# Kernel tuning notes

Hardware: AMD Instinct MI355X
Metric: run time of the kernel (lower is better)

## Reference

```python
import jax, jax.numpy as jnp
import numpy as np

B, S, D_ENC, D_DEC, UNITS = 64, 2048, 512, 512, 512


def setup_inputs() -> dict:
    key = jax.random.key(0)
    ks = jax.random.split(key, 8)
    enc = jax.random.normal(ks[0], (B, S, D_ENC), dtype=jnp.float32)
    dec = jax.random.normal(ks[1], (B, D_DEC), dtype=jnp.float32)
    # Dense params (glorot-ish scale)
    W1 = jax.random.normal(ks[2], (D_ENC, UNITS), dtype=jnp.float32) / np.sqrt(D_ENC)
    b1 = jnp.zeros((UNITS,), dtype=jnp.float32)
    W2 = jax.random.normal(ks[3], (D_DEC, UNITS), dtype=jnp.float32) / np.sqrt(D_DEC)
    b2 = jnp.zeros((UNITS,), dtype=jnp.float32)
    V = jax.random.normal(ks[4], (UNITS, 1), dtype=jnp.float32) / np.sqrt(UNITS)
    bv = jnp.zeros((1,), dtype=jnp.float32)
    return {"encoder_outputs": enc, "decoder_hidden": dec,
            "W1": W1, "b1": b1, "W2": W2, "b2": b2, "V": V, "bv": bv}


def reference(encoder_outputs, decoder_hidden, W1, b1, W2, b2, V, bv):
    # score_features: [B,S,U] = tanh(W1(enc) + W2(dec)[:,None,:])
    proj_enc = jnp.einsum('bsd,du->bsu', encoder_outputs, W1) + b1
    proj_dec = decoder_hidden @ W2 + b2                      # [B,U]
    feat = jnp.tanh(proj_enc + proj_dec[:, None, :])         # [B,S,U]
    score = jnp.einsum('bsu,uo->bso', feat, V) + bv          # [B,S,1]
    attn = jax.nn.softmax(score, axis=1)                     # softmax over seq
    context = jnp.sum(attn * encoder_outputs, axis=1)        # [B,D_enc]
    return context, jnp.squeeze(attn, axis=-1)
```

## Files before the change

### kernel.cpp

```cpp
#include <hip/hip_runtime.h>
#include <hip/hip_bf16.h>

#define BATCH 64
#define SEQ   2048
#define DIM   512
#define MROWS (BATCH * SEQ)

typedef short bf16x8 __attribute__((ext_vector_type(8)));
typedef float f32x4  __attribute__((ext_vector_type(4)));

static __device__ __forceinline__ unsigned short f2bf(float f) {
    union { float f; unsigned u; } v; v.f = f;
    unsigned u = v.u;
    u += 0x7FFFu + ((u >> 16) & 1u);
    return (unsigned short)(u >> 16);
}
static __device__ __forceinline__ float bf2f(unsigned short h) {
    union { unsigned u; float f; } v; v.u = ((unsigned)h) << 16; return v.f;
}

static __device__ __forceinline__ float tanh_fast(float x) {
    float xc = fminf(20.0f, fmaxf(-20.0f, x));
#if __has_builtin(__builtin_amdgcn_exp2f)
    float t = __builtin_amdgcn_exp2f(2.885390082f * xc);
#else
    float t = exp2f(2.885390082f * xc);
#endif
#if __has_builtin(__builtin_amdgcn_rcpf)
    return (t - 1.0f) * __builtin_amdgcn_rcpf(t + 1.0f);
#else
    return (t - 1.0f) / (t + 1.0f);
#endif
}

typedef __attribute__((address_space(1))) const unsigned int gu32;
typedef __attribute__((address_space(3))) unsigned int lu32;
static __device__ __forceinline__ void gload_lds16(const unsigned short* g,
                                                   unsigned short* l) {
    __builtin_amdgcn_global_load_lds((gu32*)g, (lu32*)l, 16, 0, 0);
}

__global__ void prep_w1t_kernel(const float* __restrict__ W1,
                                unsigned short* __restrict__ w1t) {
    int stride = gridDim.x * blockDim.x;
    for (int i = blockIdx.x * blockDim.x + threadIdx.x; i < DIM * DIM; i += stride) {
        int k = i >> 9;
        int u = i & 511;
        w1t[u * DIM + k] = f2bf(W1[i]);
    }
}

__global__ void conv_enc_kernel(const float* __restrict__ enc,
                                unsigned short* __restrict__ encb) {
    const size_t nunits = (size_t)MROWS * DIM / 8;
    size_t stride = (size_t)gridDim.x * blockDim.x;
    for (size_t u = (size_t)blockIdx.x * blockDim.x + threadIdx.x; u < nunits;
         u += stride) {
        const float4* p = (const float4*)(enc + u * 8);
        float4 a = p[0], b = p[1];
        union { ushort4 s[2]; uint4 q; } o;
        o.s[0].x = f2bf(a.x); o.s[0].y = f2bf(a.y);
        o.s[0].z = f2bf(a.z); o.s[0].w = f2bf(a.w);
        o.s[1].x = f2bf(b.x); o.s[1].y = f2bf(b.y);
        o.s[1].z = f2bf(b.z); o.s[1].w = f2bf(b.w);
        *(uint4*)(encb + u * 8) = o.q;
    }
}

__global__ void proj_dec_kernel(const float* __restrict__ dec,
                                const float* __restrict__ W2,
                                const float* __restrict__ b1,
                                const float* __restrict__ b2,
                                float* __restrict__ pd) {
    __shared__ float sdec[DIM];
    const int b = blockIdx.x;
    const int t = threadIdx.x;
    sdec[t]       = dec[b * DIM + t];
    sdec[t + 256] = dec[b * DIM + t + 256];
    __syncthreads();
    const int u0 = t, u1 = t + 256;
    float a0 = b1[u0] + b2[u0];
    float a1 = b1[u1] + b2[u1];
    for (int k = 0; k < DIM; ++k) {
        float dk = sdec[k];
        a0 += dk * W2[k * DIM + u0];
        a1 += dk * W2[k * DIM + u1];
    }
    pd[b * DIM + u0] = a0;
    pd[b * DIM + u1] = a1;
}

#define BM3 64
#define BK3 64

__global__ __launch_bounds__(256, 2) void gemm_score_v3(
    const unsigned short* __restrict__ encb,
    const unsigned short* __restrict__ w1t,
    const float* __restrict__ pd,
    const float* __restrict__ V,
    float* __restrict__ scores)
{
    __shared__ unsigned short sA[BM3 * BK3];
    __shared__ unsigned short sB[DIM * BK3];

    const int tid  = threadIdx.x;
    const int lane = tid & 63;
    const int wave = tid >> 6;
    const int quad = lane >> 4;
    const int l15  = lane & 15;

    const int row0 = blockIdx.x * BM3;

    f32x4 acc[8][4];
    for (int j = 0; j < 8; ++j)
        for (int tr = 0; tr < 4; ++tr)
            acc[j][tr] = (f32x4){0.f, 0.f, 0.f, 0.f};

    for (int k0 = 0; k0 < DIM; k0 += BK3) {
        for (int i = 0; i < 2; ++i) {
            int c  = i * 256 + tid;
            int r  = c >> 3;
            int cc = c & 7;
            int gc = cc ^ (r & 7);
            gload_lds16(encb + (size_t)(row0 + r) * DIM + k0 + gc * 8, &sA[c * 8]);
        }
        for (int i = 0; i < 16; ++i) {
            int c  = i * 256 + tid;
            int r  = c >> 3;
            int cc = c & 7;
            int gc = cc ^ (r & 7);
            gload_lds16(w1t + (size_t)r * DIM + k0 + gc * 8, &sB[c * 8]);
        }
        __syncthreads();

        for (int kk = 0; kk < BK3; kk += 32) {
            int jc = (kk >> 3) + quad;
            bf16x8 af[4];
            for (int tr = 0; tr < 4; ++tr) {
                int am = tr * 16 + l15;
                af[tr] = *(const bf16x8*)(&sA[am * BK3 + ((jc ^ (am & 7)) * 8)]);
            }
            for (int j = 0; j < 8; ++j) {
                int u = wave * 128 + j * 16 + l15;
                bf16x8 bfr = *(const bf16x8*)(&sB[u * BK3 + ((jc ^ (u & 7)) * 8)]);
                for (int tr = 0; tr < 4; ++tr)
                    acc[j][tr] = __builtin_amdgcn_mfma_f32_16x16x32_bf16(
                        af[tr], bfr, acc[j][tr], 0, 0, 0);
            }
        }
        __syncthreads();
    }

    const int b = row0 >> 11;
    float sacc[4][4];
    for (int tr = 0; tr < 4; ++tr)
        for (int r = 0; r < 4; ++r) sacc[tr][r] = 0.f;

    for (int j = 0; j < 8; ++j) {
        int u_g   = wave * 128 + j * 16 + l15;
        float pdv = pd[b * DIM + u_g];
        float vv  = V[u_g];
        for (int tr = 0; tr < 4; ++tr)
            for (int r = 0; r < 4; ++r)
                sacc[tr][r] += tanh_fast(acc[j][tr][r] + pdv) * vv;
    }
    for (int tr = 0; tr < 4; ++tr)
        for (int r = 0; r < 4; ++r) {
            float v = sacc[tr][r];
            v += __shfl_xor(v, 1);
            v += __shfl_xor(v, 2);
            v += __shfl_xor(v, 4);
            v += __shfl_xor(v, 8);
            sacc[tr][r] = v;
        }
    float* red = (float*)sA;
    if (l15 == 0) {
        for (int tr = 0; tr < 4; ++tr)
            for (int r = 0; r < 4; ++r)
                red[wave * BM3 + tr * 16 + quad * 4 + r] = sacc[tr][r];
    }
    __syncthreads();
    if (tid < BM3) {
        float s = red[tid] + red[BM3 + tid] + red[2 * BM3 + tid] + red[3 * BM3 + tid];
        scores[row0 + tid] = s;
    }
}

#define BM 128
#define BN 128
#define BK 64
#define SAS 72
__global__ __launch_bounds__(256, 2) void gemm_score_kernel(
    const float* __restrict__ enc,
    const unsigned short* __restrict__ w1t,
    const float* __restrict__ pd,
    const float* __restrict__ V,
    float* __restrict__ scores)
{
    __shared__ unsigned short sA[BM * SAS];
    __shared__ unsigned short sB[BN * SAS];

    const int tid  = threadIdx.x;
    const int lane = tid & 63;
    const int wave = tid >> 6;
    const int wm   = wave & 1;
    const int wn   = wave >> 1;
    const int quad = lane >> 4;
    const int l15  = lane & 15;

    const int row0 = blockIdx.x * BM;
    const int col0 = blockIdx.y * BN;

    f32x4 acc[4][4];
    for (int i = 0; i < 4; ++i)
        for (int j = 0; j < 4; ++j)
            acc[i][j] = (f32x4){0.f, 0.f, 0.f, 0.f};

    for (int k0 = 0; k0 < DIM; k0 += BK) {
        for (int i = 0; i < 8; ++i) {
            int s  = i * 256 + tid;
            int r  = s >> 4;
            int c4 = s & 15;
            const float4 v = *(const float4*)(enc + (size_t)(row0 + r) * DIM + k0 + c4 * 4);
            ushort4 p;
            p.x = f2bf(v.x); p.y = f2bf(v.y); p.z = f2bf(v.z); p.w = f2bf(v.w);
            *(ushort4*)(&sA[r * SAS + c4 * 4]) = p;
        }
        for (int i = 0; i < 4; ++i) {
            int s  = i * 256 + tid;
            int u  = s >> 3;
            int c8 = s & 7;
            const uint4 w = *(const uint4*)(w1t + (size_t)(col0 + u) * DIM + k0 + c8 * 8);
            *(uint4*)(&sB[u * SAS + c8 * 8]) = w;
        }
        __syncthreads();

        for (int kk = 0; kk < BK; kk += 32) {
            bf16x8 af[4], bfr[4];
            for (int t4 = 0; t4 < 4; ++t4) {
                int am = wm * 64 + t4 * 16 + l15;
                af[t4]  = *(const bf16x8*)(&sA[am * SAS + kk + quad * 8]);
                int bn = wn * 64 + t4 * 16 + l15;
                bfr[t4] = *(const bf16x8*)(&sB[bn * SAS + kk + quad * 8]);
            }
            for (int tr = 0; tr < 4; ++tr)
                for (int tc = 0; tc < 4; ++tc)
                    acc[tr][tc] = __builtin_amdgcn_mfma_f32_16x16x32_bf16(
                        af[tr], bfr[tc], acc[tr][tc], 0, 0, 0);
        }
        __syncthreads();
    }

    const int b = row0 >> 11;
    float sacc[4][4];
    for (int tr = 0; tr < 4; ++tr)
        for (int r = 0; r < 4; ++r) sacc[tr][r] = 0.f;

    for (int tc = 0; tc < 4; ++tc) {
        int u_g   = col0 + wn * 64 + tc * 16 + l15;
        float pdv = pd[b * DIM + u_g];
        float vv  = V[u_g];
        for (int tr = 0; tr < 4; ++tr)
            for (int r = 0; r < 4; ++r)
                sacc[tr][r] += tanh_fast(acc[tr][tc][r] + pdv) * vv;
    }
    for (int tr = 0; tr < 4; ++tr)
        for (int r = 0; r < 4; ++r) {
            float v = sacc[tr][r];
            v += __shfl_xor(v, 1);
            v += __shfl_xor(v, 2);
            v += __shfl_xor(v, 4);
            v += __shfl_xor(v, 8);
            sacc[tr][r] = v;
        }
    if (l15 == 0) {
        for (int tr = 0; tr < 4; ++tr)
            for (int r = 0; r < 4; ++r) {
                int m_g = row0 + wm * 64 + tr * 16 + quad * 4 + r;
                atomicAdd(&scores[m_g], sacc[tr][r]);
            }
    }
}

__global__ void softmax_kernel(const float* __restrict__ scores,
                               float* __restrict__ attn) {
    __shared__ float se[SEQ];
    __shared__ float red[256];
    const int b = blockIdx.x;
    const int t = threadIdx.x;
    const float* sc = scores + (size_t)b * SEQ;

    float v[8];
    float mx = -1e30f;
    for (int i = 0; i < 8; ++i) {
        v[i] = sc[t + i * 256];
        mx = fmaxf(mx, v[i]);
    }
    red[t] = mx;
    __syncthreads();
    for (int off = 128; off > 0; off >>= 1) {
        if (t < off) red[t] = fmaxf(red[t], red[t + off]);
        __syncthreads();
    }
    mx = red[0];
    __syncthreads();

    float sum = 0.f;
    for (int i = 0; i < 8; ++i) {
        float e = expf(v[i] - mx);
        se[t + i * 256] = e;
        sum += e;
    }
    red[t] = sum;
    __syncthreads();
    for (int off = 128; off > 0; off >>= 1) {
        if (t < off) red[t] += red[t + off];
        __syncthreads();
    }
    const float inv = 1.0f / red[0];
    for (int i = 0; i < 8; ++i)
        attn[(size_t)b * SEQ + t + i * 256] = se[t + i * 256] * inv;
}

#define SCHUNK 64
__global__ void context_fast(const unsigned short* __restrict__ encb,
                             const float* __restrict__ attn,
                             float* __restrict__ ctx) {
    __shared__ float sa[SCHUNK];
    __shared__ float sred[256 * 8];
    const int c = blockIdx.x;
    const int b = blockIdx.y;
    const int t = threadIdx.x;
    if (t < SCHUNK) sa[t] = attn[(size_t)b * SEQ + c * SCHUNK + t];
    __syncthreads();
    const int j2 = t >> 6;
    const int d0 = (t & 63) * 8;
    float a[8];
    for (int q = 0; q < 8; ++q) a[q] = 0.f;
    const unsigned short* base = encb + ((size_t)b * SEQ + (size_t)c * SCHUNK) * DIM;
    for (int it = 0; it < SCHUNK / 4; ++it) {
        int j = it * 4 + j2;
        float w = sa[j];
        bf16x8 v = *(const bf16x8*)(base + (size_t)j * DIM + d0);
        for (int q = 0; q < 8; ++q)
            a[q] += w * bf2f((unsigned short)v[q]);
    }
    for (int q = 0; q < 8; ++q) sred[t * 8 + q] = a[q];
    __syncthreads();
    if (t < 64) {
        for (int q = 0; q < 8; ++q) {
            float s = sred[t * 8 + q] + sred[(t + 64) * 8 + q] +
                      sred[(t + 128) * 8 + q] + sred[(t + 192) * 8 + q];
            atomicAdd(&ctx[b * DIM + t * 8 + q], s);
        }
    }
}

__global__ void context_kernel(const float* __restrict__ enc,
                               const float* __restrict__ attn,
                               float* __restrict__ ctx) {
    __shared__ float sa[SCHUNK];
    const int c = blockIdx.x;
    const int b = blockIdx.y;
    const int t = threadIdx.x;
    if (t < SCHUNK) sa[t] = attn[(size_t)b * SEQ + c * SCHUNK + t];
    __syncthreads();
    float a0 = 0.f, a1 = 0.f;
    const float* base = enc + ((size_t)b * SEQ + (size_t)c * SCHUNK) * DIM;
    for (int j = 0; j < SCHUNK; ++j) {
        float w = sa[j];
        a0 += w * base[(size_t)j * DIM + t];
        a1 += w * base[(size_t)j * DIM + t + 256];
    }
    atomicAdd(&ctx[b * DIM + t], a0);
    atomicAdd(&ctx[b * DIM + t + 256], a1);
}

extern "C" void kernel_launch(void* const* d_in, const int* in_sizes, int n_in,
                              void* d_out, int out_size, void* d_ws, size_t ws_size,
                              hipStream_t stream) {
    const float* enc = (const float*)d_in[0];
    const float* dec = (const float*)d_in[1];
    const float* W1  = (const float*)d_in[2];
    const float* b1  = (const float*)d_in[3];
    const float* W2  = (const float*)d_in[4];
    const float* b2  = (const float*)d_in[5];
    const float* V   = (const float*)d_in[6];

    float* out  = (float*)d_out;
    float* ctx  = out;
    float* attn = out + BATCH * DIM;

    const size_t ENCB_BYTES = (size_t)MROWS * DIM * 2;
    const size_t need = ENCB_BYTES + 131072 + 524288 + 524288;

    char* ws = (char*)d_ws;

    if (ws_size >= need) {
        unsigned short* encb = (unsigned short*)ws;
        float* pd            = (float*)(ws + ENCB_BYTES);
        unsigned short* w1t  = (unsigned short*)(ws + ENCB_BYTES + 131072);
        float* scores        = (float*)(ws + ENCB_BYTES + 131072 + 524288);

        hipMemsetAsync(ctx, 0, (size_t)BATCH * DIM * 4, stream);

        prep_w1t_kernel<<<256, 256, 0, stream>>>(W1, w1t);
        proj_dec_kernel<<<BATCH, 256, 0, stream>>>(dec, W2, b1, b2, pd);
        conv_enc_kernel<<<4096, 256, 0, stream>>>(enc, encb);
        gemm_score_v3<<<MROWS / BM3, 256, 0, stream>>>(encb, w1t, pd, V, scores);
        softmax_kernel<<<BATCH, 256, 0, stream>>>(scores, attn);
        context_fast<<<dim3(SEQ / SCHUNK, BATCH), 256, 0, stream>>>(encb, attn, ctx);
    } else {
        float* pd            = (float*)ws;
        unsigned short* w1t  = (unsigned short*)(ws + 131072);
        float* scores        = (float*)(ws + 131072 + 524288);

        hipMemsetAsync(scores, 0, (size_t)MROWS * 4, stream);
        hipMemsetAsync(ctx, 0, (size_t)BATCH * DIM * 4, stream);

        prep_w1t_kernel<<<256, 256, 0, stream>>>(W1, w1t);
        proj_dec_kernel<<<BATCH, 256, 0, stream>>>(dec, W2, b1, b2, pd);
        gemm_score_kernel<<<dim3(MROWS / BM, DIM / BN), 256, 0, stream>>>(
            enc, w1t, pd, V, scores);
        softmax_kernel<<<BATCH, 256, 0, stream>>>(scores, attn);
        context_kernel<<<dim3(SEQ / SCHUNK, BATCH), 256, 0, stream>>>(enc, attn, ctx);
    }
}
```

Baseline: 559.2 us.

## Fuse bf16 conversion into score GEMM and softmax into context kernel

```diff
diff --git a/kernel.cpp b/kernel.cpp
--- a/kernel.cpp
+++ b/kernel.cpp
@@ -14,9 +14,6 @@
     unsigned u = v.u;
     u += 0x7FFFu + ((u >> 16) & 1u);
     return (unsigned short)(u >> 16);
-}
-static __device__ __forceinline__ float bf2f(unsigned short h) {
-    union { unsigned u; float f; } v; v.u = ((unsigned)h) << 16; return v.f;
 }
 
 static __device__ __forceinline__ float tanh_fast(float x) {
@@ -50,51 +47,40 @@
     }
 }
 
-__global__ void conv_enc_kernel(const float* __restrict__ enc,
-                                unsigned short* __restrict__ encb) {
-    const size_t nunits = (size_t)MROWS * DIM / 8;
-    size_t stride = (size_t)gridDim.x * blockDim.x;
-    for (size_t u = (size_t)blockIdx.x * blockDim.x + threadIdx.x; u < nunits;
-         u += stride) {
-        const float4* p = (const float4*)(enc + u * 8);
-        float4 a = p[0], b = p[1];
-        union { ushort4 s[2]; uint4 q; } o;
-        o.s[0].x = f2bf(a.x); o.s[0].y = f2bf(a.y);
-        o.s[0].z = f2bf(a.z); o.s[0].w = f2bf(a.w);
-        o.s[1].x = f2bf(b.x); o.s[1].y = f2bf(b.y);
-        o.s[1].z = f2bf(b.z); o.s[1].w = f2bf(b.w);
-        *(uint4*)(encb + u * 8) = o.q;
-    }
-}
-
-__global__ void proj_dec_kernel(const float* __restrict__ dec,
-                                const float* __restrict__ W2,
-                                const float* __restrict__ b1,
-                                const float* __restrict__ b2,
-                                float* __restrict__ pd) {
+__global__ void proj_dec_v2(const float* __restrict__ dec,
+                            const float* __restrict__ W2,
+                            const float* __restrict__ b1,
+                            const float* __restrict__ b2,
+                            float* __restrict__ pd) {
     __shared__ float sdec[DIM];
-    const int b = blockIdx.x;
-    const int t = threadIdx.x;
+    __shared__ float red[4 * 64];
+    const int ug = blockIdx.x;
+    const int b  = blockIdx.y;
+    const int t  = threadIdx.x;
     sdec[t]       = dec[b * DIM + t];
     sdec[t + 256] = dec[b * DIM + t + 256];
     __syncthreads();
-    const int u0 = t, u1 = t + 256;
-    float a0 = b1[u0] + b2[u0];
-    float a1 = b1[u1] + b2[u1];
-    for (int k = 0; k < DIM; ++k) {
-        float dk = sdec[k];
-        a0 += dk * W2[k * DIM + u0];
-        a1 += dk * W2[k * DIM + u1];
-    }
-    pd[b * DIM + u0] = a0;
-    pd[b * DIM + u1] = a1;
+    const int u  = ug * 64 + (t & 63);
+    const int kq = t >> 6;
+    float acc = 0.f;
+    #pragma unroll 4
+    for (int k = kq * 128; k < kq * 128 + 128; ++k)
+        acc += sdec[k] * W2[k * DIM + u];
+    red[kq * 64 + (t & 63)] = acc;
+    __syncthreads();
+    if (t < 64) {
+        int u_g = ug * 64 + t;
+        float s = red[t] + red[64 + t] + red[128 + t] + red[192 + t]
+                + b1[u_g] + b2[u_g];
+        pd[b * DIM + u_g] = s;
+    }
 }
 
 #define BM3 64
 #define BK3 64
 
-__global__ __launch_bounds__(256, 2) void gemm_score_v3(
-    const unsigned short* __restrict__ encb,
+__global__ __launch_bounds__(256, 2) void gemm_score_v4(
+    const float* __restrict__ enc,
     const unsigned short* __restrict__ w1t,
     const float* __restrict__ pd,
     const float* __restrict__ V,
@@ -117,19 +103,26 @@
             acc[j][tr] = (f32x4){0.f, 0.f, 0.f, 0.f};
 
     for (int k0 = 0; k0 < DIM; k0 += BK3) {
-        for (int i = 0; i < 2; ++i) {
-            int c  = i * 256 + tid;
-            int r  = c >> 3;
-            int cc = c & 7;
-            int gc = cc ^ (r & 7);
-            gload_lds16(encb + (size_t)(row0 + r) * DIM + k0 + gc * 8, &sA[c * 8]);
-        }
         for (int i = 0; i < 16; ++i) {
             int c  = i * 256 + tid;
             int r  = c >> 3;
             int cc = c & 7;
             int gc = cc ^ (r & 7);
             gload_lds16(w1t + (size_t)r * DIM + k0 + gc * 8, &sB[c * 8]);
+        }
+        for (int i = 0; i < 2; ++i) {
+            int c  = i * 256 + tid;
+            int r  = c >> 3;
+            int cc = c & 7;
+            const float4* p =
+                (const float4*)(enc + (size_t)(row0 + r) * DIM + k0 + cc * 8);
+            float4 va = p[0], vb = p[1];
+            union { ushort4 s[2]; uint4 q; } o;
+            o.s[0].x = f2bf(va.x); o.s[0].y = f2bf(va.y);
+            o.s[0].z = f2bf(va.z); o.s[0].w = f2bf(va.w);
+            o.s[1].x = f2bf(vb.x); o.s[1].y = f2bf(vb.y);
+            o.s[1].z = f2bf(vb.z); o.s[1].w = f2bf(vb.w);
+            *(uint4*)(&sA[r * BK3 + ((cc ^ (r & 7)) * 8)]) = o.q;
         }
         __syncthreads();
 
@@ -186,110 +179,18 @@
     }
 }
 
-#define BM 128
-#define BN 128
-#define BK 64
-#define SAS 72
-__global__ __launch_bounds__(256, 2) void gemm_score_kernel(
+__global__ __launch_bounds__(256) void softmax_context_kernel(
+    const float* __restrict__ scores,
     const float* __restrict__ enc,
-    const unsigned short* __restrict__ w1t,
-    const float* __restrict__ pd,
-    const float* __restrict__ V,
-    float* __restrict__ scores)
-{
-    __shared__ unsigned short sA[BM * SAS];
-    __shared__ unsigned short sB[BN * SAS];
-
-    const int tid  = threadIdx.x;
-    const int lane = tid & 63;
-    const int wave = tid >> 6;
-    const int wm   = wave & 1;
-    const int wn   = wave >> 1;
-    const int quad = lane >> 4;
-    const int l15  = lane & 15;
-
-    const int row0 = blockIdx.x * BM;
-    const int col0 = blockIdx.y * BN;
-
-    f32x4 acc[4][4];
-    for (int i = 0; i < 4; ++i)
-        for (int j = 0; j < 4; ++j)
-            acc[i][j] = (f32x4){0.f, 0.f, 0.f, 0.f};
-
-    for (int k0 = 0; k0 < DIM; k0 += BK) {
-        for (int i = 0; i < 8; ++i) {
-            int s  = i * 256 + tid;
-            int r  = s >> 4;
-            int c4 = s & 15;
-            const float4 v = *(const float4*)(enc + (size_t)(row0 + r) * DIM + k0 + c4 * 4);
-            ushort4 p;
-            p.x = f2bf(v.x); p.y = f2bf(v.y); p.z = f2bf(v.z); p.w = f2bf(v.w);
-            *(ushort4*)(&sA[r * SAS + c4 * 4]) = p;
-        }
-        for (int i = 0; i < 4; ++i) {
-            int s  = i * 256 + tid;
-            int u  = s >> 3;
-            int c8 = s & 7;
-            const uint4 w = *(const uint4*)(w1t + (size_t)(col0 + u) * DIM + k0 + c8 * 8);
-            *(uint4*)(&sB[u * SAS + c8 * 8]) = w;
-        }
-        __syncthreads();
-
-        for (int kk = 0; kk < BK; kk += 32) {
-            bf16x8 af[4], bfr[4];
-            for (int t4 = 0; t4 < 4; ++t4) {
-                int am = wm * 64 + t4 * 16 + l15;
-                af[t4]  = *(const bf16x8*)(&sA[am * SAS + kk + quad * 8]);
-                int bn = wn * 64 + t4 * 16 + l15;
-                bfr[t4] = *(const bf16x8*)(&sB[bn * SAS + kk + quad * 8]);
-            }
-            for (int tr = 0; tr < 4; ++tr)
-                for (int tc = 0; tc < 4; ++tc)
-                    acc[tr][tc] = __builtin_amdgcn_mfma_f32_16x16x32_bf16(
-                        af[tr], bfr[tc], acc[tr][tc], 0, 0, 0);
-        }
-        __syncthreads();
-    }
-
-    const int b = row0 >> 11;
-    float sacc[4][4];
-    for (int tr = 0; tr < 4; ++tr)
-        for (int r = 0; r < 4; ++r) sacc[tr][r] = 0.f;
-
-    for (int tc = 0; tc < 4; ++tc) {
-        int u_g   = col0 + wn * 64 + tc * 16 + l15;
-        float pdv = pd[b * DIM + u_g];
-        float vv  = V[u_g];
-        for (int tr = 0; tr < 4; ++tr)
-            for (int r = 0; r < 4; ++r)
-                sacc[tr][r] += tanh_fast(acc[tr][tc][r] + pdv) * vv;
-    }
-    for (int tr = 0; tr < 4; ++tr)
-        for (int r = 0; r < 4; ++r) {
-            float v = sacc[tr][r];
-            v += __shfl_xor(v, 1);
-            v += __shfl_xor(v, 2);
-            v += __shfl_xor(v, 4);
-            v += __shfl_xor(v, 8);
-            sacc[tr][r] = v;
-        }
-    if (l15 == 0) {
-        for (int tr = 0; tr < 4; ++tr)
-            for (int r = 0; r < 4; ++r) {
-                int m_g = row0 + wm * 64 + tr * 16 + quad * 4 + r;
-                atomicAdd(&scores[m_g], sacc[tr][r]);
-            }
-    }
-}
-
-__global__ void softmax_kernel(const float* __restrict__ scores,
-                               float* __restrict__ attn) {
-    __shared__ float se[SEQ];
-    __shared__ float red[256];
-    const int b = blockIdx.x;
-    const int t = threadIdx.x;
+    float* __restrict__ attn,
+    float* __restrict__ ctx) {
+    __shared__ float sa[SEQ];
+    __shared__ float red[32 * 64];
+    const int dchunk = blockIdx.x;
+    const int b      = blockIdx.y;
+    const int t      = threadIdx.x;
+
     const float* sc = scores + (size_t)b * SEQ;
-
     float v[8];
     float mx = -1e30f;
     for (int i = 0; i < 8; ++i) {
@@ -304,11 +205,10 @@
     }
     mx = red[0];
     __syncthreads();
-
     float sum = 0.f;
     for (int i = 0; i < 8; ++i) {
         float e = expf(v[i] - mx);
-        se[t + i * 256] = e;
+        sa[t + i * 256] = e;
         sum += e;
     }
     red[t] = sum;
@@ -318,62 +218,34 @@
         __syncthreads();
     }
     const float inv = 1.0f / red[0];
-    for (int i = 0; i < 8; ++i)
-        attn[(size_t)b * SEQ + t + i * 256] = se[t + i * 256] * inv;
-}
-
-#define SCHUNK 64
-__global__ void context_fast(const unsigned short* __restrict__ encb,
-                             const float* __restrict__ attn,
-                             float* __restrict__ ctx) {
-    __shared__ float sa[SCHUNK];
-    __shared__ float sred[256 * 8];
-    const int c = blockIdx.x;
-    const int b = blockIdx.y;
-    const int t = threadIdx.x;
-    if (t < SCHUNK) sa[t] = attn[(size_t)b * SEQ + c * SCHUNK + t];
-    __syncthreads();
-    const int j2 = t >> 6;
-    const int d0 = (t & 63) * 8;
+    __syncthreads();
+    for (int i = 0; i < 8; ++i) sa[t + i * 256] *= inv;
+    if (dchunk == 0) {
+        for (int i = 0; i < 8; ++i)
+            attn[(size_t)b * SEQ + t + i * 256] = sa[t + i * 256];
+    }
+    __syncthreads();
+
+    const int tl = t & 7;
+    const int rg = t >> 3;
+    const float* base = enc + (size_t)b * SEQ * DIM + dchunk * 64 + tl * 8;
     float a[8];
     for (int q = 0; q < 8; ++q) a[q] = 0.f;
-    const unsigned short* base = encb + ((size_t)b * SEQ + (size_t)c * SCHUNK) * DIM;
-    for (int it = 0; it < SCHUNK / 4; ++it) {
-        int j = it * 4 + j2;
-        float w = sa[j];
-        bf16x8 v = *(const bf16x8*)(base + (size_t)j * DIM + d0);
-        for (int q = 0; q < 8; ++q)
-            a[q] += w * bf2f((unsigned short)v[q]);
-    }
-    for (int q = 0; q < 8; ++q) sred[t * 8 + q] = a[q];
+    for (int i = 0; i < 64; ++i) {
+        int r = rg + i * 32;
+        float w = sa[r];
+        const float4* p = (const float4*)(base + (size_t)r * DIM);
+        float4 x = p[0], y = p[1];
+        a[0] += w * x.x; a[1] += w * x.y; a[2] += w * x.z; a[3] += w * x.w;
+        a[4] += w * y.x; a[5] += w * y.y; a[6] += w * y.z; a[7] += w * y.w;
+    }
+    for (int q = 0; q < 8; ++q) red[rg * 64 + tl * 8 + q] = a[q];
     __syncthreads();
     if (t < 64) {
-        for (int q = 0; q < 8; ++q) {
-            float s = sred[t * 8 + q] + sred[(t + 64) * 8 + q] +
-                      sred[(t + 128) * 8 + q] + sred[(t + 192) * 8 + q];
-            atomicAdd(&ctx[b * DIM + t * 8 + q], s);
-        }
-    }
-}
-
-__global__ void context_kernel(const float* __restrict__ enc,
-                               const float* __restrict__ attn,
-                               float* __restrict__ ctx) {
-    __shared__ float sa[SCHUNK];
-    const int c = blockIdx.x;
-    const int b = blockIdx.y;
-    const int t = threadIdx.x;
-    if (t < SCHUNK) sa[t] = attn[(size_t)b * SEQ + c * SCHUNK + t];
-    __syncthreads();
-    float a0 = 0.f, a1 = 0.f;
-    const float* base = enc + ((size_t)b * SEQ + (size_t)c * SCHUNK) * DIM;
-    for (int j = 0; j < SCHUNK; ++j) {
-        float w = sa[j];
-        a0 += w * base[(size_t)j * DIM + t];
-        a1 += w * base[(size_t)j * DIM + t + 256];
-    }
-    atomicAdd(&ctx[b * DIM + t], a0);
-    atomicAdd(&ctx[b * DIM + t + 256], a1);
+        float s = 0.f;
+        for (int g = 0; g < 32; ++g) s += red[g * 64 + t];
+        ctx[(size_t)b * DIM + dchunk * 64 + t] = s;
+    }
 }
 
 extern "C" void kernel_launch(void* const* d_in, const int* in_sizes, int n_in,
@@ -391,38 +263,13 @@
     float* ctx  = out;
     float* attn = out + BATCH * DIM;
 
-    const size_t ENCB_BYTES = (size_t)MROWS * DIM * 2;
-    const size_t need = ENCB_BYTES + 131072 + 524288 + 524288;
-
     char* ws = (char*)d_ws;
-
-    if (ws_size >= need) {
-        unsigned short* encb = (unsigned short*)ws;
-        float* pd            = (float*)(ws + ENCB_BYTES);
-        unsigned short* w1t  = (unsigned short*)(ws + ENCB_BYTES + 131072);
-        float* scores        = (float*)(ws + ENCB_BYTES + 131072 + 524288);
-
-        hipMemsetAsync(ctx, 0, (size_t)BATCH * DIM * 4, stream);
-
-        prep_w1t_kernel<<<256, 256, 0, stream>>>(W1, w1t);
-        proj_dec_kernel<<<BATCH, 256, 0, stream>>>(dec, W2, b1, b2, pd);
-        conv_enc_kernel<<<4096, 256, 0, stream>>>(enc, encb);
-        gemm_score_v3<<<MROWS / BM3, 256, 0, stream>>>(encb, w1t, pd, V, scores);
-        softmax_kernel<<<BATCH, 256, 0, stream>>>(scores, attn);
-        context_fast<<<dim3(SEQ / SCHUNK, BATCH), 256, 0, stream>>>(encb, attn, ctx);
-    } else {
-        float* pd            = (float*)ws;
-        unsigned short* w1t  = (unsigned short*)(ws + 131072);
-        float* scores        = (float*)(ws + 131072 + 524288);
-
-        hipMemsetAsync(scores, 0, (size_t)MROWS * 4, stream);
-        hipMemsetAsync(ctx, 0, (size_t)BATCH * DIM * 4, stream);
-
-        prep_w1t_kernel<<<256, 256, 0, stream>>>(W1, w1t);
-        proj_dec_kernel<<<BATCH, 256, 0, stream>>>(dec, W2, b1, b2, pd);
-        gemm_score_kernel<<<dim3(MROWS / BM, DIM / BN), 256, 0, stream>>>(
-            enc, w1t, pd, V, scores);
-        softmax_kernel<<<BATCH, 256, 0, stream>>>(scores, attn);
-        context_kernel<<<dim3(SEQ / SCHUNK, BATCH), 256, 0, stream>>>(enc, attn, ctx);
-    }
-}
+    float* pd            = (float*)ws;
+    unsigned short* w1t  = (unsigned short*)(ws + 131072);
+    float* scores        = (float*)(ws + 131072 + 524288);
+
+    prep_w1t_kernel<<<256, 256, 0, stream>>>(W1, w1t);
+    proj_dec_v2<<<dim3(8, BATCH), 256, 0, stream>>>(dec, W2, b1, b2, pd);
+    gemm_score_v4<<<MROWS / BM3, 256, 0, stream>>>(enc, w1t, pd, V, scores);
+    softmax_context_kernel<<<dim3(8, BATCH), 256, 0, stream>>>(scores, enc, attn, ctx);
+}
```

New measurement: 468.1 us. 16.3% less time.
